# Performance work log

Hardware: AMD Instinct MI355X
Metric: run time of the kernel (lower is better)

The kernel has to match this reference:

```python
import jax, jax.numpy as jnp
import numpy as np

SIZE = 26
TEMPERATURE = 1.0
NUM_SINKHORN_ITERS = 50
EPS = 1e-8


def sinkhorn_normalize(m):
    # 50 iterations of alternating row/column normalization (doubly stochastic)
    def body(m, _):
        m = m / (jnp.sum(m, axis=1, keepdims=True) + EPS)
        m = m / (jnp.sum(m, axis=0, keepdims=True) + EPS)
        return m, None
    m, _ = jax.lax.scan(body, m, None, length=NUM_SINKHORN_ITERS)
    return m


def setup_inputs() -> dict:
    key = jax.random.key(0)
    k0, k1, k2, k3, k4, k5 = jax.random.split(key, 6)
    B, S, D = 32, 2048, 512
    input_encoding = jax.random.normal(k0, (B, S, D), dtype=jnp.float32)
    logits = jax.random.normal(k1, (SIZE, SIZE), dtype=jnp.float32)
    # nn.Linear(512, 26): weight [26, 512], bias [26]
    fp_w = jax.random.normal(k2, (SIZE, D), dtype=jnp.float32) * 0.04
    fp_b = jax.random.normal(k3, (SIZE,), dtype=jnp.float32) * 0.01
    # nn.Linear(26, 512): weight [512, 26], bias [512]
    op_w = jax.random.normal(k4, (D, SIZE), dtype=jnp.float32) * 0.15
    op_b = jax.random.normal(k5, (D,), dtype=jnp.float32) * 0.01
    return {"input_encoding": input_encoding, "logits": logits,
            "fp_w": fp_w, "fp_b": fp_b, "op_w": op_w, "op_b": op_b}


def reference(input_encoding, logits, fp_w, fp_b, op_w, op_b):
    # feature_projection: [B,S,512] -> [B,S,26]
    projected = jnp.einsum('bsd,kd->bsk', input_encoding, fp_w) + fp_b
    # soft permutation matrix
    soft_perm = sinkhorn_normalize(jax.nn.softmax(logits / TEMPERATURE, axis=-1))
    # permuted = projected @ P.T
    permuted = jnp.einsum('bsk,jk->bsj', projected, soft_perm)
    # output_projection: [B,S,26] -> [B,S,512]
    output = jnp.einsum('bsj,dj->bsd', permuted, op_w) + op_b
    return output
```

## Files before the change

kernel.cpp:

```cpp
#include <hip/hip_runtime.h>
#include <stdint.h>

#define PSIZE 26
#define DDIM  512
#define NTOK  65536
#define NIT   50
#define SEPS  1e-8f

#define BM 128
#define BN 128
#define BK 32

typedef __attribute__((ext_vector_type(4))) float f4;
typedef __attribute__((ext_vector_type(8))) short s8;

__device__ __forceinline__ unsigned short f2bf(float f) {
    unsigned int u = __builtin_bit_cast(unsigned int, f);
    u = u + 0x7fffu + ((u >> 16) & 1u);
    return (unsigned short)(u >> 16);
}

__global__ void perm_sinkhorn_kernel(const float* __restrict__ logits,
                                     const float* __restrict__ fp_b,
                                     float* __restrict__ P_out,
                                     float* __restrict__ pb_out)
{
    __shared__ float P[PSIZE][PSIZE];
    const int l = threadIdx.x;
    if (l < PSIZE) {
        float v[PSIZE];
        float mx = -1e30f;
        #pragma unroll
        for (int c = 0; c < PSIZE; ++c) { v[c] = logits[l * PSIZE + c]; mx = fmaxf(mx, v[c]); }
        float s = 0.f;
        #pragma unroll
        for (int c = 0; c < PSIZE; ++c) { v[c] = expf(v[c] - mx); s += v[c]; }
        float inv = 1.f / s;
        #pragma unroll
        for (int c = 0; c < PSIZE; ++c) P[l][c] = v[c] * inv;
    }
    __syncthreads();
    for (int it = 0; it < NIT; ++it) {
        if (l < PSIZE) {
            float s = 0.f;
            #pragma unroll
            for (int c = 0; c < PSIZE; ++c) s += P[l][c];
            float inv = 1.f / (s + SEPS);
            #pragma unroll
            for (int c = 0; c < PSIZE; ++c) P[l][c] *= inv;
        }
        __syncthreads();
        if (l < PSIZE) {
            float s = 0.f;
            #pragma unroll
            for (int r = 0; r < PSIZE; ++r) s += P[r][l];
            float inv = 1.f / (s + SEPS);
            #pragma unroll
            for (int r = 0; r < PSIZE; ++r) P[r][l] *= inv;
        }
        __syncthreads();
    }
    if (l < PSIZE) {
        float s = 0.f;
        #pragma unroll
        for (int k = 0; k < PSIZE; ++k) s += P[l][k] * fp_b[k];
        pb_out[l] = s;
        #pragma unroll
        for (int c = 0; c < PSIZE; ++c) P_out[l * PSIZE + c] = P[l][c];
    }
}

__global__ __launch_bounds__(512)
void weff_kernel(const float* __restrict__ fp_w,
                 const float* __restrict__ op_w,
                 const float* __restrict__ op_b,
                 const float* __restrict__ Pm,
                 const float* __restrict__ pb,
                 unsigned short* __restrict__ Wt,
                 float* __restrict__ beff)
{
    const int n = blockIdx.x;
    const int t = threadIdx.x;
    __shared__ float ow[PSIZE];
    __shared__ float g[PSIZE];
    if (t < PSIZE) ow[t] = op_w[n * PSIZE + t];
    __syncthreads();
    if (t < PSIZE) {
        float s = 0.f;
        #pragma unroll
        for (int j = 0; j < PSIZE; ++j) s += ow[j] * Pm[j * PSIZE + t];
        g[t] = s;
    }
    __syncthreads();
    float acc = 0.f;
    #pragma unroll
    for (int k = 0; k < PSIZE; ++k) acc += g[k] * fp_w[k * DDIM + t];
    Wt[(size_t)n * DDIM + t] = f2bf(acc);
    if (t == 0) {
        float s = 0.f;
        #pragma unroll
        for (int j = 0; j < PSIZE; ++j) s += pb[j] * ow[j];
        beff[n] = s + op_b[n];
    }
}

__global__ __launch_bounds__(256)
void gemm_kernel(const float* __restrict__ X,
                 const unsigned short* __restrict__ Wt,
                 const float* __restrict__ beff,
                 float* __restrict__ Out)
{
    __shared__ alignas(16) unsigned short Al[BM][BK];
    __shared__ alignas(16) unsigned short Bl[BN][BK];

    const int bid = blockIdx.x;
    const int lg = (bid & 7) * 256 + (bid >> 3);
    const int nb = lg & 3;
    const int mb = lg >> 2;
    const int m_base = mb * BM;
    const int n_base = nb * BN;

    const int t    = threadIdx.x;
    const int lane = t & 63;
    const int w    = t >> 6;
    const int wr   = w >> 1;
    const int wc   = w & 1;
    const int fr   = lane & 15;
    const int fc   = lane >> 4;

    f4 acc[4][4];
    #pragma unroll
    for (int i = 0; i < 4; ++i)
        #pragma unroll
        for (int j = 0; j < 4; ++j)
            acc[i][j] = (f4){0.f, 0.f, 0.f, 0.f};

    const int ar = t >> 1;
    const int ac = (t & 1) * 16;
    const float* Ag = X + (size_t)(m_base + ar) * DDIM + ac;

    unsigned short* BlBase0 = &Bl[0][0] + (size_t)(w * 64) * 8;
    unsigned short* BlBase1 = &Bl[0][0] + (size_t)(256 + w * 64) * 8;
    const int c0 = t;
    const int c1 = 256 + t;
    const unsigned short* Bg0 = Wt + (size_t)(n_base + (c0 >> 2)) * DDIM + (c0 & 3) * 8;
    const unsigned short* Bg1 = Wt + (size_t)(n_base + (c1 >> 2)) * DDIM + (c1 & 3) * 8;

    for (int kt = 0; kt < DDIM / BK; ++kt) {
        const int k0 = kt * BK;
        f4 av0 = *(const f4*)(Ag + k0 + 0);
        f4 av1 = *(const f4*)(Ag + k0 + 4);
        f4 av2 = *(const f4*)(Ag + k0 + 8);
        f4 av3 = *(const f4*)(Ag + k0 + 12);

        __syncthreads();

        __builtin_amdgcn_global_load_lds(
            (const __attribute__((address_space(1))) void*)(Bg0 + k0),
            (__attribute__((address_space(3))) void*)BlBase0, 16, 0, 0);
        __builtin_amdgcn_global_load_lds(
            (const __attribute__((address_space(1))) void*)(Bg1 + k0),
            (__attribute__((address_space(3))) void*)BlBase1, 16, 0, 0);

        s8 p0, p1;
        p0[0] = (short)f2bf(av0[0]); p0[1] = (short)f2bf(av0[1]);
        p0[2] = (short)f2bf(av0[2]); p0[3] = (short)f2bf(av0[3]);
        p0[4] = (short)f2bf(av1[0]); p0[5] = (short)f2bf(av1[1]);
        p0[6] = (short)f2bf(av1[2]); p0[7] = (short)f2bf(av1[3]);
        p1[0] = (short)f2bf(av2[0]); p1[1] = (short)f2bf(av2[1]);
        p1[2] = (short)f2bf(av2[2]); p1[3] = (short)f2bf(av2[3]);
        p1[4] = (short)f2bf(av3[0]); p1[5] = (short)f2bf(av3[1]);
        p1[6] = (short)f2bf(av3[2]); p1[7] = (short)f2bf(av3[3]);
        *(s8*)&Al[ar][ac]     = p0;
        *(s8*)&Al[ar][ac + 8] = p1;

        __syncthreads();

        s8 afr[4], bfr[4];
        #pragma unroll
        for (int mi = 0; mi < 4; ++mi)
            afr[mi] = *(const s8*)&Al[wr * 64 + mi * 16 + fr][fc * 8];
        #pragma unroll
        for (int ni = 0; ni < 4; ++ni)
            bfr[ni] = *(const s8*)&Bl[wc * 64 + ni * 16 + fr][fc * 8];
        #pragma unroll
        for (int mi = 0; mi < 4; ++mi)
            #pragma unroll
            for (int ni = 0; ni < 4; ++ni)
                acc[mi][ni] = __builtin_amdgcn_mfma_f32_16x16x32_bf16(
                    afr[mi], bfr[ni], acc[mi][ni], 0, 0, 0);
    }

    const int col0 = n_base + wc * 64 + fr;
    const int row0 = m_base + wr * 64 + fc * 4;
    #pragma unroll
    for (int ni = 0; ni < 4; ++ni) {
        const int col = col0 + ni * 16;
        const float bias = beff[col];
        #pragma unroll
        for (int mi = 0; mi < 4; ++mi) {
            const int rb = row0 + mi * 16;
            #pragma unroll
            for (int r = 0; r < 4; ++r) {
                Out[(size_t)(rb + r) * DDIM + col] = acc[mi][ni][r] + bias;
            }
        }
    }
}

extern "C" void kernel_launch(void* const* d_in, const int* in_sizes, int n_in,
                              void* d_out, int out_size, void* d_ws, size_t ws_size,
                              hipStream_t stream) {
    const float* X      = (const float*)d_in[0];
    const float* logits = (const float*)d_in[1];
    const float* fp_w   = (const float*)d_in[2];
    const float* fp_b   = (const float*)d_in[3];
    const float* op_w   = (const float*)d_in[4];
    const float* op_b   = (const float*)d_in[5];
    float* out = (float*)d_out;

    char* ws = (char*)d_ws;
    unsigned short* Wt = (unsigned short*)ws;
    float* beff = (float*)(ws + 524288);
    float* Pm   = (float*)(ws + 524288 + 4096);
    float* pb   = (float*)(ws + 524288 + 8192);

    perm_sinkhorn_kernel<<<1, 64, 0, stream>>>(logits, fp_b, Pm, pb);
    weff_kernel<<<512, 512, 0, stream>>>(fp_w, op_w, op_b, Pm, pb, Wt, beff);
    gemm_kernel<<<2048, 256, 0, stream>>>(X, Wt, beff, out);
}
```

Measured before the change: 329.0 us.

## Swizzle LDS tiles, pre-tile Wt, prefetch A, vector Sinkhorn scaling

The weight matrix is written pre-tiled and XOR-swizzled, so each k-tile is a contiguous block, and both A and B LDS tiles use a matching XOR swizzle to reduce bank conflicts on fragment reads. The A tile for the next k step is loaded from global memory during the MFMA work, and the bf16 conversion uses the packed v_cvt_pk_bf16_f32 instruction. The Sinkhorn kernel now iterates u/v scaling vectors with wavefront shuffles instead of rescaling the shared matrix with barriers. The prefetch adds register pressure, and the scaling-vector form changes rounding slightly.

New measurement: 317.5 us. 1.04x faster.

```diff
diff --git a/kernel.cpp b/kernel.cpp
--- a/kernel.cpp
+++ b/kernel.cpp
@@ -25,48 +25,53 @@
                                      float* __restrict__ P_out,
                                      float* __restrict__ pb_out)
 {
-    __shared__ float P[PSIZE][PSIZE];
+    __shared__ float Sh[PSIZE][PSIZE + 1];
     const int l = threadIdx.x;
+    float s[PSIZE];
+    float st[PSIZE];
+    #pragma unroll
+    for (int c = 0; c < PSIZE; ++c) { s[c] = 0.f; st[c] = 0.f; }
+
     if (l < PSIZE) {
-        float v[PSIZE];
         float mx = -1e30f;
         #pragma unroll
-        for (int c = 0; c < PSIZE; ++c) { v[c] = logits[l * PSIZE + c]; mx = fmaxf(mx, v[c]); }
-        float s = 0.f;
-        #pragma unroll
-        for (int c = 0; c < PSIZE; ++c) { v[c] = expf(v[c] - mx); s += v[c]; }
-        float inv = 1.f / s;
-        #pragma unroll
-        for (int c = 0; c < PSIZE; ++c) P[l][c] = v[c] * inv;
+        for (int c = 0; c < PSIZE; ++c) { s[c] = logits[l * PSIZE + c]; mx = fmaxf(mx, s[c]); }
+        float sum = 0.f;
+        #pragma unroll
+        for (int c = 0; c < PSIZE; ++c) { s[c] = expf(s[c] - mx); sum += s[c]; }
+        float inv = 1.f / sum;
+        #pragma unroll
+        for (int c = 0; c < PSIZE; ++c) { s[c] *= inv; Sh[l][c] = s[c]; }
     }
     __syncthreads();
+    if (l < PSIZE) {
+        #pragma unroll
+        for (int i = 0; i < PSIZE; ++i) st[i] = Sh[i][l];
+    }
+
+    float u = 1.f, v = 1.f;
+    float fb = (l < PSIZE) ? fp_b[l] : 0.f;
+
     for (int it = 0; it < NIT; ++it) {
-        if (l < PSIZE) {
-            float s = 0.f;
-            #pragma unroll
-            for (int c = 0; c < PSIZE; ++c) s += P[l][c];
-            float inv = 1.f / (s + SEPS);
-            #pragma unroll
-            for (int c = 0; c < PSIZE; ++c) P[l][c] *= inv;
-        }
-        __syncthreads();
-        if (l < PSIZE) {
-            float s = 0.f;
-            #pragma unroll
-            for (int r = 0; r < PSIZE; ++r) s += P[r][l];
-            float inv = 1.f / (s + SEPS);
-            #pragma unroll
-            for (int r = 0; r < PSIZE; ++r) P[r][l] *= inv;
-        }
-        __syncthreads();
-    }
+        float sv = 0.f;
+        #pragma unroll
+        for (int k = 0; k < PSIZE; ++k) sv += s[k] * __shfl(v, k);
+        u = u / (u * sv + SEPS);
+        float stu = 0.f;
+        #pragma unroll
+        for (int i = 0; i < PSIZE; ++i) stu += st[i] * __shfl(u, i);
+        v = v / (v * stu + SEPS);
+    }
+
+    const float vf = v * fb;
     if (l < PSIZE) {
-        float s = 0.f;
-        #pragma unroll
-        for (int k = 0; k < PSIZE; ++k) s += P[l][k] * fp_b[k];
-        pb_out[l] = s;
-        #pragma unroll
-        for (int c = 0; c < PSIZE; ++c) P_out[l * PSIZE + c] = P[l][c];
+        float pbv = 0.f;
+        #pragma unroll
+        for (int k = 0; k < PSIZE; ++k) pbv += s[k] * __shfl(vf, k);
+        pb_out[l] = u * pbv;
+        #pragma unroll
+        for (int c = 0; c < PSIZE; ++c)
+            P_out[l * PSIZE + c] = u * s[c] * __shfl(v, c);
     }
 }
 
@@ -86,21 +91,29 @@
     if (t < PSIZE) ow[t] = op_w[n * PSIZE + t];
     __syncthreads();
     if (t < PSIZE) {
-        float s = 0.f;
-        #pragma unroll
-        for (int j = 0; j < PSIZE; ++j) s += ow[j] * Pm[j * PSIZE + t];
-        g[t] = s;
+        float sg = 0.f;
+        #pragma unroll
+        for (int j = 0; j < PSIZE; ++j) sg += ow[j] * Pm[j * PSIZE + t];
+        g[t] = sg;
     }
     __syncthreads();
     float acc = 0.f;
     #pragma unroll
     for (int k = 0; k < PSIZE; ++k) acc += g[k] * fp_w[k * DDIM + t];
-    Wt[(size_t)n * DDIM + t] = f2bf(acc);
+
+    const int nb  = n >> 7;
+    const int row = n & 127;
+    const int kt  = t >> 5;
+    const int kc  = (t >> 3) & 3;
+    const int e   = t & 7;
+    const int sc  = kc ^ ((row >> 1) & 3);
+    Wt[(((size_t)(nb * 16 + kt) * 512) + row * 4 + sc) * 8 + e] = f2bf(acc);
+
     if (t == 0) {
-        float s = 0.f;
-        #pragma unroll
-        for (int j = 0; j < PSIZE; ++j) s += pb[j] * ow[j];
-        beff[n] = s + op_b[n];
+        float sb = 0.f;
+        #pragma unroll
+        for (int j = 0; j < PSIZE; ++j) sb += pb[j] * ow[j];
+        beff[n] = sb + op_b[n];
     }
 }
 
@@ -127,6 +140,7 @@
     const int wc   = w & 1;
     const int fr   = lane & 15;
     const int fc   = lane >> 4;
+    const int frs  = fc ^ ((fr >> 1) & 3);
 
     f4 acc[4][4];
     #pragma unroll
@@ -135,60 +149,69 @@
         for (int j = 0; j < 4; ++j)
             acc[i][j] = (f4){0.f, 0.f, 0.f, 0.f};
 
-    const int ar = t >> 1;
-    const int ac = (t & 1) * 16;
-    const float* Ag = X + (size_t)(m_base + ar) * DDIM + ac;
-
-    unsigned short* BlBase0 = &Bl[0][0] + (size_t)(w * 64) * 8;
-    unsigned short* BlBase1 = &Bl[0][0] + (size_t)(256 + w * 64) * 8;
-    const int c0 = t;
-    const int c1 = 256 + t;
-    const unsigned short* Bg0 = Wt + (size_t)(n_base + (c0 >> 2)) * DDIM + (c0 & 3) * 8;
-    const unsigned short* Bg1 = Wt + (size_t)(n_base + (c1 >> 2)) * DDIM + (c1 & 3) * 8;
+    const int ar  = t >> 1;
+    const int acH = t & 1;
+    const float* Ag = X + (size_t)(m_base + ar) * DDIM + acH * 16;
+    const int wsc0 = (2 * acH)     ^ ((ar >> 1) & 3);
+    const int wsc1 = (2 * acH + 1) ^ ((ar >> 1) & 3);
+    unsigned short* Aw0 = &Al[ar][wsc0 * 8];
+    unsigned short* Aw1 = &Al[ar][wsc1 * 8];
+
+    unsigned short* BlB0 = &Bl[0][0] + (size_t)(w * 64) * 8;
+    unsigned short* BlB1 = &Bl[0][0] + (size_t)(256 + w * 64) * 8;
+    const unsigned short* Bg0 = Wt + (size_t)nb * 65536 + (size_t)t * 8;
+    const unsigned short* Bg1 = Wt + (size_t)nb * 65536 + (size_t)(256 + t) * 8;
+
+    f4 a0 = *(const f4*)(Ag + 0);
+    f4 a1 = *(const f4*)(Ag + 4);
+    f4 a2 = *(const f4*)(Ag + 8);
+    f4 a3 = *(const f4*)(Ag + 12);
 
     for (int kt = 0; kt < DDIM / BK; ++kt) {
-        const int k0 = kt * BK;
-        f4 av0 = *(const f4*)(Ag + k0 + 0);
-        f4 av1 = *(const f4*)(Ag + k0 + 4);
-        f4 av2 = *(const f4*)(Ag + k0 + 8);
-        f4 av3 = *(const f4*)(Ag + k0 + 12);
-
         __syncthreads();
 
         __builtin_amdgcn_global_load_lds(
-            (const __attribute__((address_space(1))) void*)(Bg0 + k0),
-            (__attribute__((address_space(3))) void*)BlBase0, 16, 0, 0);
+            (const __attribute__((address_space(1))) void*)(Bg0 + kt * 4096),
+            (__attribute__((address_space(3))) void*)BlB0, 16, 0, 0);
         __builtin_amdgcn_global_load_lds(
-            (const __attribute__((address_space(1))) void*)(Bg1 + k0),
-            (__attribute__((address_space(3))) void*)BlBase1, 16, 0, 0);
-
-        s8 p0, p1;
-        p0[0] = (short)f2bf(av0[0]); p0[1] = (short)f2bf(av0[1]);
-        p0[2] = (short)f2bf(av0[2]); p0[3] = (short)f2bf(av0[3]);
-        p0[4] = (short)f2bf(av1[0]); p0[5] = (short)f2bf(av1[1]);
-        p0[6] = (short)f2bf(av1[2]); p0[7] = (short)f2bf(av1[3]);
-        p1[0] = (short)f2bf(av2[0]); p1[1] = (short)f2bf(av2[1]);
-        p1[2] = (short)f2bf(av2[2]); p1[3] = (short)f2bf(av2[3]);
-        p1[4] = (short)f2bf(av3[0]); p1[5] = (short)f2bf(av3[1]);
-        p1[6] = (short)f2bf(av3[2]); p1[7] = (short)f2bf(av3[3]);
-        *(s8*)&Al[ar][ac]     = p0;
-        *(s8*)&Al[ar][ac + 8] = p1;
+            (const __attribute__((address_space(1))) void*)(Bg1 + kt * 4096),
+            (__attribute__((address_space(3))) void*)BlB1, 16, 0, 0);
+
+        union { s8 v; unsigned int u[4]; } p0, p1;
+        asm("v_cvt_pk_bf16_f32 %0, %1, %2" : "=v"(p0.u[0]) : "v"(a0[0]), "v"(a0[1]));
+        asm("v_cvt_pk_bf16_f32 %0, %1, %2" : "=v"(p0.u[1]) : "v"(a0[2]), "v"(a0[3]));
+        asm("v_cvt_pk_bf16_f32 %0, %1, %2" : "=v"(p0.u[2]) : "v"(a1[0]), "v"(a1[1]));
+        asm("v_cvt_pk_bf16_f32 %0, %1, %2" : "=v"(p0.u[3]) : "v"(a1[2]), "v"(a1[3]));
+        asm("v_cvt_pk_bf16_f32 %0, %1, %2" : "=v"(p1.u[0]) : "v"(a2[0]), "v"(a2[1]));
+        asm("v_cvt_pk_bf16_f32 %0, %1, %2" : "=v"(p1.u[1]) : "v"(a2[2]), "v"(a2[3]));
+        asm("v_cvt_pk_bf16_f32 %0, %1, %2" : "=v"(p1.u[2]) : "v"(a3[0]), "v"(a3[1]));
+        asm("v_cvt_pk_bf16_f32 %0, %1, %2" : "=v"(p1.u[3]) : "v"(a3[2]), "v"(a3[3]));
+        *(s8*)Aw0 = p0.v;
+        *(s8*)Aw1 = p1.v;
 
         __syncthreads();
 
+        const float* An = Ag + ((kt < 15) ? (kt + 1) * BK : kt * BK);
+        f4 n0 = *(const f4*)(An + 0);
+        f4 n1 = *(const f4*)(An + 4);
+        f4 n2 = *(const f4*)(An + 8);
+        f4 n3 = *(const f4*)(An + 12);
+
         s8 afr[4], bfr[4];
         #pragma unroll
         for (int mi = 0; mi < 4; ++mi)
-            afr[mi] = *(const s8*)&Al[wr * 64 + mi * 16 + fr][fc * 8];
+            afr[mi] = *(const s8*)&Al[wr * 64 + mi * 16 + fr][frs * 8];
         #pragma unroll
         for (int ni = 0; ni < 4; ++ni)
-            bfr[ni] = *(const s8*)&Bl[wc * 64 + ni * 16 + fr][fc * 8];
+            bfr[ni] = *(const s8*)&Bl[wc * 64 + ni * 16 + fr][frs * 8];
         #pragma unroll
         for (int mi = 0; mi < 4; ++mi)
             #pragma unroll
             for (int ni = 0; ni < 4; ++ni)
                 acc[mi][ni] = __builtin_amdgcn_mfma_f32_16x16x32_bf16(
                     afr[mi], bfr[ni], acc[mi][ni], 0, 0, 0);
+
+        a0 = n0; a1 = n1; a2 = n2; a3 = n3;
     }
 
     const int col0 = n_base + wc * 64 + fr;
```
